# Optimization experiments

Hardware: AMD Instinct MI355X
Metric: run time of the kernel (lower is better)

The kernel has to match this reference:

```python
import jax, jax.numpy as jnp
import numpy as np

N = 100000
E = 600000
NODE_DIM = 128
EDGE_DIM = 32
HIDDEN = 128  # must equal NODE_DIM (index_add_ into zeros_like(node_features))


def _linear_params(key, fan_in, fan_out):
    kw, kb = jax.random.split(key)
    bound = 1.0 / np.sqrt(fan_in)
    W = jax.random.uniform(kw, (fan_in, fan_out), minval=-bound, maxval=bound, dtype=jnp.float32)
    b = jax.random.uniform(kb, (fan_out,), minval=-bound, maxval=bound, dtype=jnp.float32)
    return W, b


def setup_inputs() -> dict:
    key = jax.random.key(0)
    ks = jax.random.split(key, 8)
    node_features = jax.random.normal(ks[0], (N, NODE_DIM), dtype=jnp.float32)
    edge_index = jax.random.randint(ks[1], (2, E), 0, N, dtype=jnp.int32)
    edge_features = jax.random.normal(ks[2], (E, EDGE_DIM), dtype=jnp.float32)
    m_W1, m_b1 = _linear_params(ks[3], 2 * NODE_DIM + EDGE_DIM, HIDDEN)
    m_W2, m_b2 = _linear_params(ks[4], HIDDEN, HIDDEN)
    a_W, a_b = _linear_params(ks[5], HIDDEN, 1)
    u_W1, u_b1 = _linear_params(ks[6], NODE_DIM + HIDDEN, HIDDEN)
    u_W2, u_b2 = _linear_params(ks[7], HIDDEN, NODE_DIM)
    return {
        "node_features": node_features,
        "edge_features": edge_features,
        "m_W1": m_W1, "m_b1": m_b1, "m_W2": m_W2, "m_b2": m_b2,
        "a_W": a_W, "a_b": a_b,
        "u_W1": u_W1, "u_b1": u_b1, "u_W2": u_W2, "u_b2": u_b2,
        "edge_index": edge_index,
    }


def reference(node_features, edge_features, m_W1, m_b1, m_W2, m_b2,
              a_W, a_b, u_W1, u_b1, u_W2, u_b2, edge_index):
    row, col = edge_index[0], edge_index[1]
    # gather endpoints + edge feats -> [E, 2*node_dim + edge_dim]
    msg_in = jnp.concatenate([node_features[row], node_features[col], edge_features], axis=-1)
    # message MLP
    h = jax.nn.relu(msg_in @ m_W1 + m_b1)
    messages = h @ m_W2 + m_b2  # [E, hidden]
    # global softmax over all edges (dim=0), per attention column (width 1)
    attn = jax.nn.softmax(messages @ a_W + a_b, axis=0)  # [E, 1]
    messages = messages * attn
    # scatter-add into destination nodes
    aggregated = jax.ops.segment_sum(messages, col, num_segments=node_features.shape[0])
    # update MLP + residual
    upd_in = jnp.concatenate([node_features, aggregated], axis=-1)
    u = jax.nn.relu(upd_in @ u_W1 + u_b1)
    updated = u @ u_W2 + u_b2
    return updated + node_features
```

## Files before the change

kernel.cpp:

```cpp
#include <hip/hip_runtime.h>
#include <hip/hip_bf16.h>
#include <hip/hip_fp8.h>
#include <stdint.h>

#define NN 100000
#define NE 600000
#define ND 128
#define ED 32
#define HID 128
#define SCANB 391
#define NEB 4688

using short8 = __attribute__((ext_vector_type(8))) short;
using f32x4  = __attribute__((ext_vector_type(4))) float;
using f32x2  = __attribute__((ext_vector_type(2))) float;

__device__ __forceinline__ uint32_t f2bf(float f) {
  uint32_t u = __float_as_uint(f);
  return (u + 0x7FFFu + ((u >> 16) & 1u)) >> 16;
}
__device__ __forceinline__ float bf2f(uint32_t h) {
  return __uint_as_float(h << 16);
}
__device__ __forceinline__ short8 pack8(float4 a, float4 b) {
  short8 s;
  s[0] = (short)f2bf(a.x); s[1] = (short)f2bf(a.y);
  s[2] = (short)f2bf(a.z); s[3] = (short)f2bf(a.w);
  s[4] = (short)f2bf(b.x); s[5] = (short)f2bf(b.y);
  s[6] = (short)f2bf(b.z); s[7] = (short)f2bf(b.w);
  return s;
}

__device__ __forceinline__ uint8_t fp8_enc(float v) {
#if __has_builtin(__builtin_amdgcn_cvt_pk_fp8_f32)
  return (uint8_t)(__builtin_amdgcn_cvt_pk_fp8_f32(v, v, 0, false) & 0xFF);
#else
  __hip_fp8_e4m3 q(v);
  return q.__x;
#endif
}
__device__ __forceinline__ float2 fp8_dec2(uint32_t v) {
#if __has_builtin(__builtin_amdgcn_cvt_pk_f32_fp8)
  f32x2 r = __builtin_amdgcn_cvt_pk_f32_fp8((int)v, false);
  return make_float2(r[0], r[1]);
#else
  __hip_fp8_e4m3 qa, qb;
  qa.__x = (uint8_t)(v & 0xFF); qb.__x = (uint8_t)((v >> 8) & 0xFF);
  return make_float2((float)qa, (float)qb);
#endif
}
__device__ __forceinline__ long pack_fp8x8(float4 a, float4 b) {
  union { uint8_t u8[8]; long l; } u;
  u.u8[0] = fp8_enc(a.x); u.u8[1] = fp8_enc(a.y);
  u.u8[2] = fp8_enc(a.z); u.u8[3] = fp8_enc(a.w);
  u.u8[4] = fp8_enc(b.x); u.u8[5] = fp8_enc(b.y);
  u.u8[6] = fp8_enc(b.z); u.u8[7] = fp8_enc(b.w);
  return u.l;
}

__global__ __launch_bounds__(256) void k_prep_all(
    const float* __restrict__ uW1, const float* __restrict__ uW2,
    const float* __restrict__ W1, const float* __restrict__ W2,
    short* __restrict__ U1p, short* __restrict__ U2p,
    uint8_t* __restrict__ W1p8, uint8_t* __restrict__ W2p8,
    int* __restrict__ cnt, int* __restrict__ counter) {
  int o = blockIdx.x * 256 + threadIdx.x;
  if (o < NN) cnt[o] = 0;
  if (o == 0) *counter = 0;
  const float* src; int rel; int isFp8;
  short* dstS = nullptr; uint8_t* dst8 = nullptr;
  if (o < 32768)       { rel = o;         src = uW1; dstS = U1p;  isFp8 = 0; }
  else if (o < 49152)  { rel = o - 32768; src = uW2; dstS = U2p;  isFp8 = 0; }
  else if (o < 86016)  { rel = o - 49152; src = W1;  dst8 = W1p8; isFp8 = 1; }
  else if (o < 102400) { rel = o - 86016; src = W2;  dst8 = W2p8; isFp8 = 1; }
  else return;
  int j = rel & 7, c16 = (rel >> 3) & 15, g = (rel >> 7) & 3, nt = (rel >> 9) & 7, c = rel >> 12;
  int k = c * 32 + g * 8 + j, n = nt * 16 + c16;
  float v = src[k * 128 + n];
  if (isFp8) dst8[rel] = fp8_enc(v);
  else       dstS[rel] = (short)f2bf(v);
}

__global__ __launch_bounds__(256) void k_prep_nf(const float* __restrict__ nf,
                                                 short* __restrict__ nfb,
                                                 uint8_t* __restrict__ nfb8,
                                                 const int* __restrict__ ei,
                                                 int* __restrict__ cnt) {
  const int total = NN * ND / 8;
  int gid = blockIdx.x * 256 + threadIdx.x;
  for (int e = gid; e < NE; e += gridDim.x * 256)
    atomicAdd(&cnt[ei[NE + e]], 1);
  for (int u = gid; u < total; u += gridDim.x * 256) {
    const float* s = nf + (size_t)u * 8;
    float4 v0 = *(const float4*)s, v1 = *(const float4*)(s + 4);
    *(short8*)(nfb + (size_t)u * 8) = pack8(v0, v1);
    uint8_t b[8];
    b[0] = fp8_enc(v0.x); b[1] = fp8_enc(v0.y); b[2] = fp8_enc(v0.z); b[3] = fp8_enc(v0.w);
    b[4] = fp8_enc(v1.x); b[5] = fp8_enc(v1.y); b[6] = fp8_enc(v1.z); b[7] = fp8_enc(v1.w);
    *(uint2*)(nfb8 + (size_t)u * 8) = *(const uint2*)b;
  }
}

__global__ __launch_bounds__(256, 4) void k_edge_mfma(
    const uint8_t* __restrict__ nfb8, const float* __restrict__ ef,
    const uint8_t* __restrict__ W1p8, const float* __restrict__ b1,
    const uint8_t* __restrict__ W2p8, const float* __restrict__ b2,
    const float* __restrict__ aW, const int* __restrict__ ei,
    const int* __restrict__ perm,
    uint8_t* __restrict__ msg8, float* __restrict__ logits) {
  __shared__ __align__(16) uint8_t sRow[128 * 136];
  __shared__ __align__(16) uint8_t sCol[128 * 136];
  __shared__ __align__(16) uint8_t sB8[4096];
  __shared__ int sIdx[256];
  __shared__ int sPerm[128];

  const int tid = threadIdx.x;
  const int wv = tid >> 6, ln = tid & 63, cr = ln & 15, gp = ln >> 4;
  const int e0 = blockIdx.x * 128;
  const int wrow = wv * 32;

  if (tid < 128) {
    int e = e0 + tid; if (e >= NE) e = NE - 1;
    sIdx[tid] = ei[e];
    sIdx[128 + tid] = ei[NE + e];
    sPerm[tid] = perm[e];
  }
  __syncthreads();

#pragma unroll
  for (int it = 0; it < 16; ++it) {
    int t = it * 256 + tid;
    int side = t >> 11;
    int r = (t & 2047) >> 4;
    int o = (t & 15) * 8;
    const uint8_t* src = nfb8 + (size_t)sIdx[side * 128 + r] * ND + o;
    uint8_t* dst = (side ? sCol : sRow) + r * 136 + o;
    *(uint2*)dst = *(const uint2*)src;
  }

  long efA0, efA1;
  {
    int ea = e0 + wrow + cr;      if (ea >= NE) ea = NE - 1;
    int eb = e0 + wrow + 16 + cr; if (eb >= NE) eb = NE - 1;
    const float* f0 = ef + (size_t)ea * ED + gp * 8;
    const float* f1 = ef + (size_t)eb * ED + gp * 8;
    efA0 = pack_fp8x8(*(const float4*)f0, *(const float4*)(f0 + 4));
    efA1 = pack_fp8x8(*(const float4*)f1, *(const float4*)(f1 + 4));
  }

  float bia[8], aWr[8], bia2[8];
#pragma unroll
  for (int nt = 0; nt < 8; ++nt) {
    bia[nt] = b1[nt * 16 + cr];
    bia2[nt] = b2[nt * 16 + cr];
    aWr[nt] = aW[nt * 16 + cr];
  }
  f32x4 acc[2][8];
#pragma unroll
  for (int mt = 0; mt < 2; ++mt)
#pragma unroll
    for (int nt = 0; nt < 8; ++nt)
      acc[mt][nt] = (f32x4){bia[nt], bia[nt], bia[nt], bia[nt]};

  for (int c = 0; c < 9; ++c) {
    __syncthreads();
    *(uint4*)&sB8[tid * 16] = *(const uint4*)(W1p8 + c * 4096 + tid * 16);
    __syncthreads();
    long af0, af1;
    if (c < 8) {
      const uint8_t* aSrc = (c < 4) ? (sRow + c * 32) : (sCol + (c - 4) * 32);
      af0 = *(const long*)(aSrc + (wrow + cr) * 136 + gp * 8);
      af1 = *(const long*)(aSrc + (wrow + 16 + cr) * 136 + gp * 8);
    } else {
      af0 = efA0; af1 = efA1;
    }
#pragma unroll
    for (int nt = 0; nt < 8; ++nt) {
      long bfr = *(const long*)&sB8[(nt * 4 + gp) * 128 + cr * 8];
      acc[0][nt] = __builtin_amdgcn_mfma_f32_16x16x32_fp8_fp8(af0, bfr, acc[0][nt], 0, 0, 0);
      acc[1][nt] = __builtin_amdgcn_mfma_f32_16x16x32_fp8_fp8(af1, bfr, acc[1][nt], 0, 0, 0);
    }
  }

#pragma unroll
  for (int mt = 0; mt < 2; ++mt)
#pragma unroll
    for (int nt = 0; nt < 8; ++nt)
#pragma unroll
      for (int rr = 0; rr < 4; ++rr)
        sRow[(wrow + mt * 16 + gp * 4 + rr) * 136 + nt * 16 + cr] =
            fp8_enc(fmaxf(acc[mt][nt][rr], 0.f));

  f32x4 acc2[2][8];
#pragma unroll
  for (int mt = 0; mt < 2; ++mt)
#pragma unroll
    for (int nt = 0; nt < 8; ++nt)
      acc2[mt][nt] = (f32x4){bia2[nt], bia2[nt], bia2[nt], bia2[nt]};
  for (int c2 = 0; c2 < 4; ++c2) {
    __syncthreads();
    *(uint4*)&sB8[tid * 16] = *(const uint4*)(W2p8 + c2 * 4096 + tid * 16);
    __syncthreads();
    long af0 = *(const long*)&sRow[(wrow + cr) * 136 + c2 * 32 + gp * 8];
    long af1 = *(const long*)&sRow[(wrow + 16 + cr) * 136 + c2 * 32 + gp * 8];
#pragma unroll
    for (int nt = 0; nt < 8; ++nt) {
      long bfr = *(const long*)&sB8[(nt * 4 + gp) * 128 + cr * 8];
      acc2[0][nt] = __builtin_amdgcn_mfma_f32_16x16x32_fp8_fp8(af0, bfr, acc2[0][nt], 0, 0, 0);
      acc2[1][nt] = __builtin_amdgcn_mfma_f32_16x16x32_fp8_fp8(af1, bfr, acc2[1][nt], 0, 0, 0);
    }
  }

#pragma unroll
  for (int mt = 0; mt < 2; ++mt)
#pragma unroll
    for (int rr = 0; rr < 4; ++rr) {
      float p = 0.f;
#pragma unroll
      for (int nt = 0; nt < 8; ++nt) p += acc2[mt][nt][rr] * aWr[nt];
      p += __shfl_xor(p, 1, 64);
      p += __shfl_xor(p, 2, 64);
      p += __shfl_xor(p, 4, 64);
      p += __shfl_xor(p, 8, 64);
      int row = wrow + mt * 16 + gp * 4 + rr;
      if (cr == 0 && e0 + row < NE) logits[sPerm[row]] = p;
    }

#pragma unroll
  for (int mt = 0; mt < 2; ++mt)
#pragma unroll
    for (int nt = 0; nt < 8; ++nt)
#pragma unroll
      for (int rr = 0; rr < 4; ++rr)
        sCol[(wrow + mt * 16 + gp * 4 + rr) * 136 + nt * 16 + cr] =
            fp8_enc(acc2[mt][nt][rr]);
  __syncthreads();
#pragma unroll
  for (int it = 0; it < 8; ++it) {
    int row = it * 16 + (tid >> 4), o8 = (tid & 15) * 8;
    if (e0 + row < NE)
      *(uint2*)(msg8 + (size_t)sPerm[row] * HID + o8) = *(const uint2*)&sCol[row * 136 + o8];
  }
}

__global__ __launch_bounds__(256, 4) void k_node_fused(
    const short* __restrict__ nfb, const uint8_t* __restrict__ msg8,
    const float* __restrict__ logits, const int* __restrict__ rowptr,
    const float* __restrict__ red,
    const short* __restrict__ U1p, const float* __restrict__ b1,
    const short* __restrict__ U2p, const float* __restrict__ b2,
    float* __restrict__ out) {
  __shared__ __align__(16) short sBuf[128 * 136];

  const int tid = threadIdx.x;
  const int wv = tid >> 6, ln = tid & 63, cr = ln & 15, gp = ln >> 4;
  const int n0 = blockIdx.x * 128;
  const int wrow = wv * 32;
  const float gm = red[0], inv = red[1];

  for (int j = 0; j < 32; ++j) {
    int n = n0 + wrow + j;
    if (n >= NN) break;
    int i0 = rowptr[n], i1 = rowptr[n + 1];
    float a0 = 0.f, a1 = 0.f;
    for (int i = i0; i < i1; ++i) {
      float wt = expf(logits[i] - gm) * inv;
      uint32_t pk = *(const uint16_t*)(msg8 + (size_t)i * HID + ln * 2);
      float2 d = fp8_dec2(pk);
      a0 += wt * d.x;
      a1 += wt * d.y;
    }
    uint32_t packed = f2bf(a0) | (f2bf(a1) << 16);
    *(uint32_t*)&sBuf[(wrow + j) * 136 + ln * 2] = packed;
  }

  int na0 = n0 + wrow + cr;      if (na0 >= NN) na0 = NN - 1;
  int na1 = n0 + wrow + 16 + cr; if (na1 >= NN) na1 = NN - 1;

  float bia[8], bia2[8];
#pragma unroll
  for (int nt = 0; nt < 8; ++nt) {
    bia[nt] = b1[nt * 16 + cr];
    bia2[nt] = b2[nt * 16 + cr];
  }
  f32x4 acc[2][8];
#pragma unroll
  for (int mt = 0; mt < 2; ++mt)
#pragma unroll
    for (int nt = 0; nt < 8; ++nt)
      acc[mt][nt] = (f32x4){bia[nt], bia[nt], bia[nt], bia[nt]};

#pragma unroll
  for (int c = 0; c < 8; ++c) {
    short8 af0, af1;
    if (c < 4) {
      const int ko = c * 32 + gp * 8;
      af0 = *(const short8*)(nfb + (size_t)na0 * ND + ko);
      af1 = *(const short8*)(nfb + (size_t)na1 * ND + ko);
    } else {
      const int ko = (c - 4) * 32 + gp * 8;
      af0 = *(const short8*)&sBuf[(wrow + cr) * 136 + ko];
      af1 = *(const short8*)&sBuf[(wrow + 16 + cr) * 136 + ko];
    }
    const short* Wc = U1p + c * 4096;
#pragma unroll
    for (int nt = 0; nt < 8; ++nt) {
      short8 bfr = *(const short8*)(Wc + (nt * 4 + gp) * 128 + cr * 8);
      acc[0][nt] = __builtin_amdgcn_mfma_f32_16x16x32_bf16(af0, bfr, acc[0][nt], 0, 0, 0);
      acc[1][nt] = __builtin_amdgcn_mfma_f32_16x16x32_bf16(af1, bfr, acc[1][nt], 0, 0, 0);
    }
  }

#pragma unroll
  for (int mt = 0; mt < 2; ++mt)
#pragma unroll
    for (int nt = 0; nt < 8; ++nt)
#pragma unroll
      for (int rr = 0; rr < 4; ++rr)
        sBuf[(wrow + mt * 16 + gp * 4 + rr) * 136 + nt * 16 + cr] =
            (short)f2bf(fmaxf(acc[mt][nt][rr], 0.f));

  f32x4 acc2[2][8];
#pragma unroll
  for (int mt = 0; mt < 2; ++mt)
#pragma unroll
    for (int nt = 0; nt < 8; ++nt)
      acc2[mt][nt] = (f32x4){bia2[nt], bia2[nt], bia2[nt], bia2[nt]};
#pragma unroll
  for (int c2 = 0; c2 < 4; ++c2) {
    short8 af0 = *(const short8*)&sBuf[(wrow + cr) * 136 + c2 * 32 + gp * 8];
    short8 af1 = *(const short8*)&sBuf[(wrow + 16 + cr) * 136 + c2 * 32 + gp * 8];
    const short* Wc = U2p + c2 * 4096;
#pragma unroll
    for (int nt = 0; nt < 8; ++nt) {
      short8 bfr = *(const short8*)(Wc + (nt * 4 + gp) * 128 + cr * 8);
      acc2[0][nt] = __builtin_amdgcn_mfma_f32_16x16x32_bf16(af0, bfr, acc2[0][nt], 0, 0, 0);
      acc2[1][nt] = __builtin_amdgcn_mfma_f32_16x16x32_bf16(af1, bfr, acc2[1][nt], 0, 0, 0);
    }
  }

#pragma unroll
  for (int mt = 0; mt < 2; ++mt)
#pragma unroll
    for (int rr = 0; rr < 4; ++rr) {
      int n = n0 + wrow + mt * 16 + gp * 4 + rr;
      if (n < NN) {
#pragma unroll
        for (int nt = 0; nt < 8; ++nt) {
          int col = nt * 16 + cr;
          float r = bf2f((uint16_t)nfb[(size_t)n * ND + col]);
          out[(size_t)n * ND + col] = acc2[mt][nt][rr] + r;
        }
      }
    }
}

__device__ __forceinline__ void ms_combine(float& m, float& s, float m2, float s2) {
  float M = fmaxf(m, m2);
  s = s * expf(m - M) + s2 * expf(m2 - M);
  m = M;
}
__device__ __forceinline__ void ms_block_reduce(float& m, float& s) {
#pragma unroll
  for (int o = 1; o < 64; o <<= 1) {
    float m2 = __shfl_xor(m, o, 64), s2 = __shfl_xor(s, o, 64);
    ms_combine(m, s, m2, s2);
  }
  __shared__ float sm[4], ss[4];
  if ((threadIdx.x & 63) == 0) { sm[threadIdx.x >> 6] = m; ss[threadIdx.x >> 6] = s; }
  __syncthreads();
  m = sm[0]; s = ss[0];
  ms_combine(m, s, sm[1], ss[1]);
  ms_combine(m, s, sm[2], ss[2]);
  ms_combine(m, s, sm[3], ss[3]);
}
__global__ __launch_bounds__(256) void k_red(const float* __restrict__ logits,
                                             float* __restrict__ pmax,
                                             float* __restrict__ psum,
                                             float* __restrict__ red,
                                             int* __restrict__ counter) {
  float m = -3.402823466e38f, s = 0.f;
  for (int i = blockIdx.x * 256 + threadIdx.x; i < NE; i += 1024 * 256) {
    float l = logits[i];
    if (l <= m) s += expf(l - m);
    else { s = s * expf(m - l) + 1.f; m = l; }
  }
  ms_block_reduce(m, s);
  __shared__ int lastFlag;
  if (threadIdx.x == 0) {
    pmax[blockIdx.x] = m; psum[blockIdx.x] = s;
    __threadfence();
    lastFlag = (__hip_atomic_fetch_add(counter, 1, __ATOMIC_ACQ_REL,
                                       __HIP_MEMORY_SCOPE_AGENT) == 1023);
  }
  __syncthreads();
  if (!lastFlag) return;
  int t = threadIdx.x;
  float fm = __hip_atomic_load(&pmax[t], __ATOMIC_RELAXED, __HIP_MEMORY_SCOPE_AGENT);
  float fs = __hip_atomic_load(&psum[t], __ATOMIC_RELAXED, __HIP_MEMORY_SCOPE_AGENT);
#pragma unroll
  for (int k = 1; k < 4; ++k) {
    float m2 = __hip_atomic_load(&pmax[t + k * 256], __ATOMIC_RELAXED, __HIP_MEMORY_SCOPE_AGENT);
    float s2 = __hip_atomic_load(&psum[t + k * 256], __ATOMIC_RELAXED, __HIP_MEMORY_SCOPE_AGENT);
    ms_combine(fm, fs, m2, s2);
  }
  ms_block_reduce(fm, fs);
  if (t == 0) { red[0] = fm; red[1] = 1.0f / fs; }
}

__global__ __launch_bounds__(256) void k_scan_bsum(const int* __restrict__ cnt,
                                                   int* __restrict__ bsum) {
  int i = blockIdx.x * 256 + threadIdx.x;
  int v = (i < NN) ? cnt[i] : 0;
#pragma unroll
  for (int s = 1; s < 64; s <<= 1) v += __shfl_xor(v, s, 64);
  __shared__ int sv[4];
  if ((threadIdx.x & 63) == 0) sv[threadIdx.x >> 6] = v;
  __syncthreads();
  if (threadIdx.x == 0) bsum[blockIdx.x] = sv[0] + sv[1] + sv[2] + sv[3];
}
__global__ __launch_bounds__(512) void k_scan_boff(const int* __restrict__ bsum,
                                                   int* __restrict__ boff,
                                                   int* __restrict__ rowptr) {
  __shared__ int s[512];
  int t = threadIdx.x;
  int v = (t < SCANB) ? bsum[t] : 0;
  s[t] = v;
  __syncthreads();
  for (int off = 1; off < 512; off <<= 1) {
    int u = (t >= off) ? s[t - off] : 0;
    __syncthreads();
    s[t] += u;
    __syncthreads();
  }
  if (t < SCANB) boff[t] = s[t] - v;
  if (t == 0) rowptr[NN] = NE;
}
__global__ __launch_bounds__(256) void k_scan_final(int* __restrict__ cnt,
                                                    const int* __restrict__ boff,
                                                    int* __restrict__ rowptr) {
  __shared__ int s[256];
  int b = blockIdx.x, t = threadIdx.x, i = b * 256 + t;
  int v = (i < NN) ? cnt[i] : 0;
  s[t] = v;
  __syncthreads();
  for (int off = 1; off < 256; off <<= 1) {
    int u = (t >= off) ? s[t - off] : 0;
    __syncthreads();
    s[t] += u;
    __syncthreads();
  }
  int excl = s[t] - v + boff[b];
  if (i < NN) { rowptr[i] = excl; cnt[i] = excl; }
}
__global__ __launch_bounds__(256) void k_fill(const int* __restrict__ ei,
                                              int* __restrict__ cursor,
                                              int* __restrict__ perm) {
  int e = blockIdx.x * 256 + threadIdx.x;
  if (e >= NE) return;
  int c = ei[NE + e];
  int pos = atomicAdd(&cursor[c], 1);
  perm[e] = pos;
}

extern "C" void kernel_launch(void* const* d_in, const int* in_sizes, int n_in,
                              void* d_out, int out_size, void* d_ws, size_t ws_size,
                              hipStream_t stream) {
  const float* nf  = (const float*)d_in[0];
  const float* ef  = (const float*)d_in[1];
  const float* mW1 = (const float*)d_in[2];
  const float* mb1 = (const float*)d_in[3];
  const float* mW2 = (const float*)d_in[4];
  const float* mb2 = (const float*)d_in[5];
  const float* aW  = (const float*)d_in[6];
  const float* uW1 = (const float*)d_in[8];
  const float* ub1 = (const float*)d_in[9];
  const float* uW2 = (const float*)d_in[10];
  const float* ub2 = (const float*)d_in[11];
  const int*   ei  = (const int*)d_in[12];
  float* out = (float*)d_out;

  char* ws = (char*)d_ws;
  uint8_t* msg8 = (uint8_t*)ws;
  float* logits = (float*)(ws + 76800000);
  float* pmax = (float*)(ws + 79200000);
  float* psum = pmax + 1024;
  float* red  = psum + 1024;
  int* counter = (int*)(red + 2);
  uint8_t* W1p8 = (uint8_t*)(ws + 79208256 + 64);
  uint8_t* W2p8 = W1p8 + 36864;
  short* U1p = (short*)(W2p8 + 16384);
  short* U2p = U1p + 32768;
  int* rowptr = (int*)(ws + 79413056);
  int* cnt    = rowptr + (NN + 1);
  int* perm   = cnt + NN;
  int* bsum   = perm + NE;
  int* boff   = bsum + 512;
  short* nfb  = (short*)(ws + 82620000);
  uint8_t* nfb8 = (uint8_t*)(ws + 108220000);

  k_prep_all<<<400, 256, 0, stream>>>(uW1, uW2, mW1, mW2, U1p, U2p, W1p8, W2p8,
                                      cnt, counter);
  k_prep_nf<<<2048, 256, 0, stream>>>(nf, nfb, nfb8, ei, cnt);
  k_scan_bsum<<<SCANB, 256, 0, stream>>>(cnt, bsum);
  k_scan_boff<<<1, 512, 0, stream>>>(bsum, boff, rowptr);
  k_scan_final<<<SCANB, 256, 0, stream>>>(cnt, boff, rowptr);
  k_fill<<<(NE + 255) / 256, 256, 0, stream>>>(ei, cnt, perm);
  k_edge_mfma<<<NEB, 256, 0, stream>>>(nfb8, ef, W1p8, mb1, W2p8, mb2, aW, ei, perm,
                                       msg8, logits);
  k_red<<<1024, 256, 0, stream>>>(logits, pmax, psum, red, counter);
  k_node_fused<<<(NN + 127) / 128, 256, 0, stream>>>(nfb, msg8, logits, rowptr,
                                                     red, U1p, ub1, U2p, ub2, out);
}
```

Measured before the change: 348.3 us.

## Split node aggregation into a separate wave-per-node kernel before the update MLP

The softmax-weighted CSR gather of edge messages is moved out of the fused node kernel into its own kernel, where each wavefront handles one node. The result goes to a bf16 buffer in global memory, which the MFMA update kernel then reads as its second input half. In the fused version each wave walked 32 nodes in sequence, which gave little latency hiding for these irregular gathers. The split exposes far more parallelism, at the cost of an extra launch and a round trip of the bf16 aggregate through global memory.

```diff
diff --git a/kernel.cpp b/kernel.cpp
--- a/kernel.cpp
+++ b/kernel.cpp
@@ -243,36 +243,17 @@
   }
 }
 
-__global__ __launch_bounds__(256, 4) void k_node_fused(
-    const short* __restrict__ nfb, const uint8_t* __restrict__ msg8,
-    const float* __restrict__ logits, const int* __restrict__ rowptr,
-    const float* __restrict__ red,
+__global__ __launch_bounds__(256, 4) void k_node_mfma(
+    const short* __restrict__ nfb, const short* __restrict__ aggb,
     const short* __restrict__ U1p, const float* __restrict__ b1,
     const short* __restrict__ U2p, const float* __restrict__ b2,
     float* __restrict__ out) {
-  __shared__ __align__(16) short sBuf[128 * 136];
+  __shared__ __align__(16) short sH[128 * 136];
 
   const int tid = threadIdx.x;
   const int wv = tid >> 6, ln = tid & 63, cr = ln & 15, gp = ln >> 4;
   const int n0 = blockIdx.x * 128;
   const int wrow = wv * 32;
-  const float gm = red[0], inv = red[1];
-
-  for (int j = 0; j < 32; ++j) {
-    int n = n0 + wrow + j;
-    if (n >= NN) break;
-    int i0 = rowptr[n], i1 = rowptr[n + 1];
-    float a0 = 0.f, a1 = 0.f;
-    for (int i = i0; i < i1; ++i) {
-      float wt = expf(logits[i] - gm) * inv;
-      uint32_t pk = *(const uint16_t*)(msg8 + (size_t)i * HID + ln * 2);
-      float2 d = fp8_dec2(pk);
-      a0 += wt * d.x;
-      a1 += wt * d.y;
-    }
-    uint32_t packed = f2bf(a0) | (f2bf(a1) << 16);
-    *(uint32_t*)&sBuf[(wrow + j) * 136 + ln * 2] = packed;
-  }
 
   int na0 = n0 + wrow + cr;      if (na0 >= NN) na0 = NN - 1;
   int na1 = n0 + wrow + 16 + cr; if (na1 >= NN) na1 = NN - 1;
@@ -292,16 +273,10 @@
 
 #pragma unroll
   for (int c = 0; c < 8; ++c) {
-    short8 af0, af1;
-    if (c < 4) {
-      const int ko = c * 32 + gp * 8;
-      af0 = *(const short8*)(nfb + (size_t)na0 * ND + ko);
-      af1 = *(const short8*)(nfb + (size_t)na1 * ND + ko);
-    } else {
-      const int ko = (c - 4) * 32 + gp * 8;
-      af0 = *(const short8*)&sBuf[(wrow + cr) * 136 + ko];
-      af1 = *(const short8*)&sBuf[(wrow + 16 + cr) * 136 + ko];
-    }
+    const short* base = (c < 4) ? nfb : aggb;
+    const int ko = (c & 3) * 32 + gp * 8;
+    short8 af0 = *(const short8*)(base + (size_t)na0 * ND + ko);
+    short8 af1 = *(const short8*)(base + (size_t)na1 * ND + ko);
     const short* Wc = U1p + c * 4096;
 #pragma unroll
     for (int nt = 0; nt < 8; ++nt) {
@@ -317,7 +292,7 @@
     for (int nt = 0; nt < 8; ++nt)
 #pragma unroll
       for (int rr = 0; rr < 4; ++rr)
-        sBuf[(wrow + mt * 16 + gp * 4 + rr) * 136 + nt * 16 + cr] =
+        sH[(wrow + mt * 16 + gp * 4 + rr) * 136 + nt * 16 + cr] =
             (short)f2bf(fmaxf(acc[mt][nt][rr], 0.f));
 
   f32x4 acc2[2][8];
@@ -328,8 +303,8 @@
       acc2[mt][nt] = (f32x4){bia2[nt], bia2[nt], bia2[nt], bia2[nt]};
 #pragma unroll
   for (int c2 = 0; c2 < 4; ++c2) {
-    short8 af0 = *(const short8*)&sBuf[(wrow + cr) * 136 + c2 * 32 + gp * 8];
-    short8 af1 = *(const short8*)&sBuf[(wrow + 16 + cr) * 136 + c2 * 32 + gp * 8];
+    short8 af0 = *(const short8*)&sH[(wrow + cr) * 136 + c2 * 32 + gp * 8];
+    short8 af1 = *(const short8*)&sH[(wrow + 16 + cr) * 136 + c2 * 32 + gp * 8];
     const short* Wc = U2p + c2 * 4096;
 #pragma unroll
     for (int nt = 0; nt < 8; ++nt) {
@@ -461,6 +436,27 @@
   int c = ei[NE + e];
   int pos = atomicAdd(&cursor[c], 1);
   perm[e] = pos;
+}
+
+__global__ __launch_bounds__(256) void k_agg(
+    const uint8_t* __restrict__ msg8, const float* __restrict__ logits,
+    const int* __restrict__ rowptr, const float* __restrict__ red,
+    short* __restrict__ aggb) {
+  int n = blockIdx.x * 4 + (threadIdx.x >> 6);
+  int lane = threadIdx.x & 63;
+  if (n >= NN) return;
+  float gm = red[0], inv = red[1];
+  int i0 = rowptr[n], i1 = rowptr[n + 1];
+  float a0 = 0.f, a1 = 0.f;
+  for (int i = i0; i < i1; ++i) {
+    float wt = expf(logits[i] - gm) * inv;
+    uint32_t pk = *(const uint16_t*)(msg8 + (size_t)i * HID + lane * 2);
+    float2 d = fp8_dec2(pk);
+    a0 += wt * d.x;
+    a1 += wt * d.y;
+  }
+  uint32_t packed = f2bf(a0) | (f2bf(a1) << 16);
+  *(uint32_t*)(aggb + (size_t)n * ND + lane * 2) = packed;
 }
 
 extern "C" void kernel_launch(void* const* d_in, const int* in_sizes, int n_in,
@@ -487,7 +483,7 @@
   float* psum = pmax + 1024;
   float* red  = psum + 1024;
   int* counter = (int*)(red + 2);
-  uint8_t* W1p8 = (uint8_t*)(ws + 79208256 + 64);
+  uint8_t* W1p8 = (uint8_t*)(ws + 79208320);
   uint8_t* W2p8 = W1p8 + 36864;
   short* U1p = (short*)(W2p8 + 16384);
   short* U2p = U1p + 32768;
@@ -498,6 +494,7 @@
   int* boff   = bsum + 512;
   short* nfb  = (short*)(ws + 82620000);
   uint8_t* nfb8 = (uint8_t*)(ws + 108220000);
+  short* aggb = (short*)(ws + 121020000);
 
   k_prep_all<<<400, 256, 0, stream>>>(uW1, uW2, mW1, mW2, U1p, U2p, W1p8, W2p8,
                                       cnt, counter);
@@ -509,6 +506,6 @@
   k_edge_mfma<<<NEB, 256, 0, stream>>>(nfb8, ef, W1p8, mb1, W2p8, mb2, aW, ei, perm,
                                        msg8, logits);
   k_red<<<1024, 256, 0, stream>>>(logits, pmax, psum, red, counter);
-  k_node_fused<<<(NN + 127) / 128, 256, 0, stream>>>(nfb, msg8, logits, rowptr,
-                                                     red, U1p, ub1, U2p, ub2, out);
-}
+  k_agg<<<(NN + 3) / 4, 256, 0, stream>>>(msg8, logits, rowptr, red, aggb);
+  k_node_mfma<<<(NN + 127) / 128, 256, 0, stream>>>(nfb, aggb, U1p, ub1, U2p, ub2, out);
+}
```

After: 314.2 us. 1.11x faster.
